# Kernel optimization log

Hardware: AMD Instinct MI355X
Metric: run time of the kernel (lower is better)

Reference implementation:

```python
import jax, jax.numpy as jnp
import numpy as np

N = 50000   # nodes
E = 800000  # edges (before self-loops)
G = 512     # graphs in batch
H = 4       # heads
C = 32      # hidden dim per head
NEG = 0.2   # LeakyReLU slope in GATConv
EPS = 1e-5  # BatchNorm eps


def setup_inputs():
    k = jax.random.split(jax.random.key(0), 32)
    f = lambda i, s: 0.1 * jax.random.normal(k[i], s, dtype=jnp.float32)
    inp = {
        "x": jax.random.normal(k[0], (N, 4), dtype=jnp.float32),
        "edge_index": jax.random.randint(k[1], (2, E), 0, N, dtype=jnp.int32),
        "batch": ((jnp.arange(N) * G) // N).astype(jnp.int32),  # sorted, every graph non-empty
        "u": jax.random.normal(k[2], (G, 10), dtype=jnp.float32),
    }
    dims = [(4, H * C, H, H * C), (H * C, H * C, H, H * C), (H * C, C, 1, C)]
    j = 3
    for l, (din, dout, hh, dbn) in enumerate(dims):
        inp[f"W{l}"] = f(j, (din, dout)); j += 1
        inp[f"a_src{l}"] = f(j, (hh, C)); j += 1
        inp[f"a_dst{l}"] = f(j, (hh, C)); j += 1
        inp[f"b{l}"] = f(j, (dbn,)); j += 1
        inp[f"bn_g{l}"] = 1.0 + f(j, (dbn,)); j += 1
        inp[f"bn_b{l}"] = f(j, (dbn,)); j += 1
        inp[f"bn_m{l}"] = f(j, (dbn,)); j += 1
        inp[f"bn_v{l}"] = 1.0 + 0.1 * jax.random.uniform(k[j], (dbn,), dtype=jnp.float32); j += 1
    inp["l1w"] = f(j, (2 * C + 10, C)); j += 1
    inp["l1b"] = f(j, (C,)); j += 1
    inp["l2w"] = f(j, (C, 1)); j += 1
    inp["l2b"] = f(j, (1,)); j += 1
    return inp


def gat(x, src, dst, W, a_s, a_d, b, heads, ch, concat):
    n = x.shape[0]
    h = (x @ W).reshape(n, heads, ch)                                   # [N,H,C]
    al_s = jnp.einsum('nhc,hc->nh', h, a_s)
    al_d = jnp.einsum('nhc,hc->nh', h, a_d)
    e = jax.nn.leaky_relu(al_s[src] + al_d[dst], NEG)                   # [E',H]
    m = jax.ops.segment_max(e, dst, num_segments=n)                     # per-dst softmax
    p = jnp.exp(e - m[dst])
    alpha = p / (jax.ops.segment_sum(p, dst, num_segments=n)[dst] + 1e-16)
    out = jax.ops.segment_sum(h[src] * alpha[:, :, None], dst, num_segments=n)
    out = out.reshape(n, heads * ch) if concat else out.mean(axis=1)
    return out + b


def bn(x, g, b, m, v):  # eval-mode BatchNorm1d
    return (x - m) * jax.lax.rsqrt(v + EPS) * g + b


def reference(x, edge_index, batch, u,
              W0, a_src0, a_dst0, b0, bn_g0, bn_b0, bn_m0, bn_v0,
              W1, a_src1, a_dst1, b1, bn_g1, bn_b1, bn_m1, bn_v1,
              W2, a_src2, a_dst2, b2, bn_g2, bn_b2, bn_m2, bn_v2,
              l1w, l1b, l2w, l2b):
    loops = jnp.arange(N, dtype=edge_index.dtype)  # GATConv add_self_loops=True
    src = jnp.concatenate([edge_index[0], loops])
    dst = jnp.concatenate([edge_index[1], loops])
    x = jax.nn.elu(bn(gat(x, src, dst, W0, a_src0, a_dst0, b0, H, C, True), bn_g0, bn_b0, bn_m0, bn_v0))
    x = jax.nn.elu(bn(gat(x, src, dst, W1, a_src1, a_dst1, b1, H, C, True), bn_g1, bn_b1, bn_m1, bn_v1))
    x = jax.nn.elu(bn(gat(x, src, dst, W2, a_src2, a_dst2, b2, 1, C, False), bn_g2, bn_b2, bn_m2, bn_v2))
    cnt = jax.ops.segment_sum(jnp.ones((N,), x.dtype), batch, num_segments=G)
    x_mean = jax.ops.segment_sum(x, batch, num_segments=G) / cnt[:, None]
    x_max = jax.ops.segment_max(x, batch, num_segments=G)
    comb = jnp.concatenate([x_mean, x_max, u], axis=1)                  # [G, 2C+10]
    hid = jax.nn.relu(comb @ l1w + l1b)
    return jax.nn.sigmoid(hid @ l2w + l2b)[:, 0]                        # [G]
```

## Files before the change

### kernel.cpp

```cpp
#include <hip/hip_runtime.h>
#include <hip/hip_bf16.h>
#include <math.h>

#define LRELU_NEG 0.2f
#define BN_EPS 1e-5f
#define CSR_SHIFT 7

typedef __attribute__((ext_vector_type(8))) short bf16x8;
typedef __attribute__((ext_vector_type(4))) float f32x4;

__device__ __forceinline__ float lrelu(float x) { return x > 0.f ? x : LRELU_NEG * x; }
__device__ __forceinline__ float b2f(__hip_bfloat16 v) { return __bfloat162float(v); }
__device__ __forceinline__ unsigned short f2bu(float v) {
  __hip_bfloat16 b = __float2bfloat16(v);
  return *(unsigned short*)&b;
}
__device__ __forceinline__ float blo(unsigned int u) { return __uint_as_float(u << 16); }
__device__ __forceinline__ float bhi(unsigned int u) { return __uint_as_float(u & 0xFFFF0000u); }
__device__ __forceinline__ float elu_fast(float v) { return v > 0.f ? v : __expf(v) - 1.f; }
__device__ __forceinline__ float ldw(const void* p, int i, int fl) {
  return fl ? b2f(((const __hip_bfloat16*)p)[i]) : ((const float*)p)[i];
}

__global__ __launch_bounds__(256) void k_setup(const int* __restrict__ ei, int E, int EN, int ebks,
                                               const unsigned short* __restrict__ w, int wn,
                                               int* __restrict__ flag, int* __restrict__ ph) {
  int b = blockIdx.x;
  int tid = threadIdx.x;
  if (b == ebks) {
    __shared__ int bad_s;
    if (tid == 0) bad_s = 0;
    __syncthreads();
    int bad = 0;
    for (int i = 2 * tid; i < wn; i += 512) {
      unsigned short u = w[i];
      if ((u & 0x7FFF) == 0) continue;
      int ex = (u >> 7) & 0xFF;
      if (ex > 131 || ex < 90) bad++;
    }
    atomicAdd(&bad_s, bad);
    __syncthreads();
    if (tid == 0) *flag = (bad_s < 2048) ? 1 : 0;
    return;
  }
  __shared__ int hist[512];
  hist[tid] = 0; hist[tid + 256] = 0;
  __syncthreads();
  int base = b * 4096;
  for (int i = 0; i < 16; i++) {
    int e = base + i * 256 + tid;
    if (e < EN) {
      int dst = (e < E) ? ei[E + e] : (e - E);
      atomicAdd(&hist[dst >> CSR_SHIFT], 1);
    }
  }
  __syncthreads();
  ph[b * 512 + tid] = hist[tid];
  ph[b * 512 + tid + 256] = hist[tid + 256];
}

__global__ __launch_bounds__(512) void k_bucketscan(const int* __restrict__ ph, int ebks,
                                                    int* __restrict__ bbase, int* __restrict__ gcursor) {
  __shared__ int wpre[8];
  int tid = threadIdx.x, lane = tid & 63, wid = tid >> 6;
  int v = 0;
  for (int i = 0; i < ebks; i++) v += ph[i * 512 + tid];
  int x = v;
  #pragma unroll
  for (int off = 1; off < 64; off <<= 1) {
    int y = __shfl_up(x, off);
    if (lane >= off) x += y;
  }
  if (lane == 63) wpre[wid] = x;
  __syncthreads();
  if (tid == 0) {
    int acc = 0;
    #pragma unroll
    for (int w = 0; w < 8; w++) { int t = wpre[w]; wpre[w] = acc; acc += t; }
  }
  __syncthreads();
  int excl = wpre[wid] + x - v;
  bbase[tid] = excl;
  gcursor[tid] = excl;
  if (tid == 511) bbase[512] = excl + v;
}

__global__ __launch_bounds__(256) void k_binscatter(const int* __restrict__ ei, int* __restrict__ gcursor,
                                                    unsigned int* __restrict__ pairs, int E, int EN) {
  __shared__ int cnt[512];
  __shared__ int base[512];
  int tid = threadIdx.x;
  cnt[tid] = 0; cnt[tid + 256] = 0;
  __syncthreads();
  int eb = blockIdx.x * 4096;
  int srcs[16], dsts[16];
  #pragma unroll
  for (int i = 0; i < 16; i++) {
    int e = eb + i * 256 + tid;
    srcs[i] = -1; dsts[i] = 0;
    if (e < EN) {
      int s, d;
      if (e < E) { s = ei[e]; d = ei[E + e]; } else { s = e - E; d = s; }
      srcs[i] = s; dsts[i] = d;
      atomicAdd(&cnt[d >> CSR_SHIFT], 1);
    }
  }
  __syncthreads();
  for (int b = tid; b < 512; b += 256) {
    int c = cnt[b];
    base[b] = c ? atomicAdd(&gcursor[b], c) : 0;
    cnt[b] = 0;
  }
  __syncthreads();
  #pragma unroll
  for (int i = 0; i < 16; i++) {
    if (srcs[i] >= 0) {
      int b = dsts[i] >> CSR_SHIFT;
      int loc = atomicAdd(&cnt[b], 1);
      pairs[base[b] + loc] = ((unsigned int)srcs[i] << CSR_SHIFT) | (unsigned int)(dsts[i] & 127);
    }
  }
}

__global__ __launch_bounds__(256) void k_csrfin(const unsigned int* __restrict__ pairs,
                                                const int* __restrict__ bbase,
                                                int* __restrict__ rs, int* __restrict__ col,
                                                int N, int EN) {
  __shared__ int dcount[128];
  __shared__ int wsum;
  __shared__ int lcur[128];
  int b = blockIdx.x, tid = threadIdx.x;
  if (tid < 128) dcount[tid] = 0;
  __syncthreads();
  int s = bbase[b], e = bbase[b + 1];
  for (int i = s + tid; i < e; i += 256)
    atomicAdd(&dcount[pairs[i] & 127], 1);
  __syncthreads();
  int x = 0, v = 0, wid = 0;
  if (tid < 128) {
    v = dcount[tid];
    int lane = tid & 63; wid = tid >> 6;
    x = v;
    #pragma unroll
    for (int off = 1; off < 64; off <<= 1) {
      int y = __shfl_up(x, off);
      if (lane >= off) x += y;
    }
    if (wid == 0 && lane == 63) wsum = x;
  }
  __syncthreads();
  if (tid < 128) {
    int excl = x - v + (wid ? wsum : 0);
    int r = s + excl;
    int node = (b << CSR_SHIFT) + tid;
    if (node < N) rs[node] = r;
    lcur[tid] = r;
  }
  if (b == 0 && tid == 0) rs[N] = EN;
  __syncthreads();
  for (int i = s + tid; i < e; i += 256) {
    unsigned int p = pairs[i];
    int pos = atomicAdd(&lcur[p & 127], 1);
    col[pos] = (int)(p >> CSR_SHIFT);
  }
}

struct FoldArgs {
  const void *W0, *as0, *ad0, *W1, *as1, *ad1, *W2, *as2, *ad2;
  const void *bn[15];
  float* W0p; __hip_bfloat16* Wt1; __hip_bfloat16* Wt2;
  float *A0, *B0, *A1, *B1, *A2, *B2;
};

__global__ __launch_bounds__(256) void k_foldW(FoldArgs fa, const int* __restrict__ flag) {
  int idx = blockIdx.x * 256 + threadIdx.x;
  int fl = *flag;
  if (idx < 576) {
    int k = idx / 144, c = idx % 144;
    float v = 0.f;
    if (c < 128) v = ldw(fa.W0, k * 128 + c, fl);
    else if (c < 136) {
      int hh = (c - 128) & 3; const void* a = (c < 132) ? fa.as0 : fa.ad0;
      float s = 0.f;
      for (int cc = 0; cc < 32; cc++)
        s += ldw(fa.W0, k * 128 + hh * 32 + cc, fl) * ldw(a, hh * 32 + cc, fl);
      v = s;
    }
    fa.W0p[k * 144 + c] = v;
    return;
  }
  idx -= 576;
  if (idx < 144 * 128) {
    int c = idx >> 7, k = idx & 127;
    float v = 0.f;
    if (c < 128) v = ldw(fa.W1, k * 128 + c, fl);
    else if (c < 136) {
      int hh = (c - 128) & 3; const void* a = (c < 132) ? fa.as1 : fa.ad1;
      float s = 0.f;
      for (int cc = 0; cc < 32; cc++)
        s += ldw(fa.W1, k * 128 + hh * 32 + cc, fl) * ldw(a, hh * 32 + cc, fl);
      v = s;
    }
    fa.Wt1[c * 128 + k] = __float2bfloat16(v);
    return;
  }
  idx -= 144 * 128;
  if (idx < 48 * 128) {
    int c = idx >> 7, k = idx & 127;
    float v = 0.f;
    if (c < 32) v = ldw(fa.W2, k * 32 + c, fl);
    else if (c == 32) { float s = 0.f; for (int cc = 0; cc < 32; cc++) s += ldw(fa.W2, k * 32 + cc, fl) * ldw(fa.as2, cc, fl); v = s; }
    else if (c == 33) { float s = 0.f; for (int cc = 0; cc < 32; cc++) s += ldw(fa.W2, k * 32 + cc, fl) * ldw(fa.ad2, cc, fl); v = s; }
    fa.Wt2[c * 128 + k] = __float2bfloat16(v);
    return;
  }
  idx -= 48 * 128;
  if (idx < 128) {
    float A = ldw(fa.bn[1], idx, fl) * rsqrtf(ldw(fa.bn[4], idx, fl) + BN_EPS);
    fa.A0[idx] = A;
    fa.B0[idx] = (ldw(fa.bn[0], idx, fl) - ldw(fa.bn[3], idx, fl)) * A + ldw(fa.bn[2], idx, fl);
    return;
  }
  idx -= 128;
  if (idx < 128) {
    float A = ldw(fa.bn[6], idx, fl) * rsqrtf(ldw(fa.bn[9], idx, fl) + BN_EPS);
    fa.A1[idx] = A;
    fa.B1[idx] = (ldw(fa.bn[5], idx, fl) - ldw(fa.bn[8], idx, fl)) * A + ldw(fa.bn[7], idx, fl);
    return;
  }
  idx -= 128;
  if (idx < 32) {
    float A = ldw(fa.bn[11], idx, fl) * rsqrtf(ldw(fa.bn[14], idx, fl) + BN_EPS);
    fa.A2[idx] = A;
    fa.B2[idx] = (ldw(fa.bn[10], idx, fl) - ldw(fa.bn[13], idx, fl)) * A + ldw(fa.bn[12], idx, fl);
  }
}

__global__ __launch_bounds__(256) void k_gemm0(const void* __restrict__ x, const float* __restrict__ W0p,
    const int* __restrict__ flag,
    __hip_bfloat16* __restrict__ h, float* __restrict__ als, float* __restrict__ ald, int N) {
  int t = blockIdx.x * 256 + threadIdx.x;
  int nrow = t / 36, cg = t - nrow * 36;
  if (nrow >= N) return;
  float4 xv;
  if (*flag) {
    uint2 tv = ((const uint2*)x)[nrow];
    xv = make_float4(blo(tv.x), bhi(tv.x), blo(tv.y), bhi(tv.y));
  } else {
    xv = ((const float4*)x)[nrow];
  }
  int c0 = cg * 4;
  float o[4];
  #pragma unroll
  for (int j = 0; j < 4; j++) {
    int c = c0 + j;
    o[j] = fmaf(xv.x, W0p[c], fmaf(xv.y, W0p[144 + c], fmaf(xv.z, W0p[288 + c], xv.w * W0p[432 + c])));
  }
  if (c0 < 128) {
    uint2 pk;
    pk.x = ((unsigned int)f2bu(o[1]) << 16) | f2bu(o[0]);
    pk.y = ((unsigned int)f2bu(o[3]) << 16) | f2bu(o[2]);
    *((uint2*)((unsigned short*)h + (size_t)nrow * 128) + cg) = pk;
  } else if (c0 == 128) {
    *(float4*)(als + (size_t)nrow * 4) = make_float4(o[0], o[1], o[2], o[3]);
  } else {
    *(float4*)(ald + (size_t)nrow * 4) = make_float4(o[0], o[1], o[2], o[3]);
  }
}

template <int CT, int DOUT, int HEADS>
__global__ __launch_bounds__(256) void k_mm(const __hip_bfloat16* __restrict__ xa,
    const __hip_bfloat16* __restrict__ Wt,
    __hip_bfloat16* __restrict__ h, float* __restrict__ als, float* __restrict__ ald, int N) {
  __shared__ unsigned short A_s[64 * 128];
  __shared__ unsigned short B_s[CT * 16 * 128];
  int tid = threadIdx.x;
  int row0 = blockIdx.x * 64;

  for (int i = tid; i < 1024; i += 256) {
    int r = i >> 4, slot = i & 15;
    int gr = row0 + r;
    float4 v = make_float4(0.f, 0.f, 0.f, 0.f);
    if (gr < N) v = ((const float4*)(xa + (size_t)gr * 128))[slot];
    *(float4*)((char*)A_s + r * 256 + ((slot ^ (r & 7)) << 4)) = v;
  }
  for (int i = tid; i < CT * 256; i += 256) {
    int r = i >> 4, slot = i & 15;
    float4 v = ((const float4*)Wt)[i];
    *(float4*)((char*)B_s + r * 256 + ((slot ^ (r & 7)) << 4)) = v;
  }
  __syncthreads();

  int l = tid & 63, w = tid >> 6;
  int lr = l & 15, lg = l >> 4;
  f32x4 acc[CT];
  #pragma unroll
  for (int ct = 0; ct < CT; ct++) acc[ct] = (f32x4){0.f, 0.f, 0.f, 0.f};

  int rA = w * 16 + lr;
  #pragma unroll
  for (int k0 = 0; k0 < 4; k0++) {
    int slot = k0 * 4 + lg;
    bf16x8 a = *(const bf16x8*)((const char*)A_s + rA * 256 + ((slot ^ (rA & 7)) << 4));
    #pragma unroll
    for (int ct = 0; ct < CT; ct++) {
      int rB = ct * 16 + lr;
      bf16x8 b = *(const bf16x8*)((const char*)B_s + rB * 256 + ((slot ^ (rB & 7)) << 4));
      acc[ct] = __builtin_amdgcn_mfma_f32_16x16x32_bf16(a, b, acc[ct], 0, 0, 0);
    }
  }

  #pragma unroll
  for (int ct = 0; ct < CT; ct++) {
    #pragma unroll
    for (int j = 0; j < 4; j++) {
      int gr = row0 + w * 16 + lg * 4 + j;
      if (gr >= N) continue;
      int col = ct * 16 + lr;
      float v = acc[ct][j];
      if (col < DOUT)                 h[(size_t)gr * DOUT + col] = __float2bfloat16(v);
      else if (col < DOUT + HEADS)    als[(size_t)gr * HEADS + (col - DOUT)] = v;
      else if (col < DOUT + 2*HEADS)  ald[(size_t)gr * HEADS + (col - DOUT - HEADS)] = v;
    }
  }
}

__global__ __launch_bounds__(256) void k_agg4(const __hip_bfloat16* __restrict__ h, const float* __restrict__ als,
    const float* __restrict__ ald, const int* __restrict__ rs, const int* __restrict__ col,
    const float* __restrict__ Aarr, const float* __restrict__ Barr,
    __hip_bfloat16* __restrict__ out, int N) {
  __shared__ int svs[8][32];
  __shared__ float ps[8][32][4];
  int tid = threadIdx.x;
  int sub = tid & 31, gi = tid >> 5;
  int n = blockIdx.x * 8 + gi;
  if (n >= N) return;
  int row = rs[n], deg = rs[n + 1] - row;
  float4 ad4 = *(const float4*)(ald + (size_t)n * 4);
  int hh2 = sub >> 3;
  float acc0 = 0.f, acc1 = 0.f, acc2 = 0.f, acc3 = 0.f;
  float s0 = 0.f, s1 = 0.f, s2 = 0.f, s3 = 0.f;

  for (int base = 0; base < deg; base += 32) {
    int k = base + sub;
    int sv = 0; float q0 = 0.f, q1 = 0.f, q2 = 0.f, q3 = 0.f;
    if (k < deg) {
      sv = col[row + k];
      float4 a4 = *(const float4*)(als + (size_t)sv * 4);
      q0 = __expf(lrelu(a4.x + ad4.x));
      q1 = __expf(lrelu(a4.y + ad4.y));
      q2 = __expf(lrelu(a4.z + ad4.z));
      q3 = __expf(lrelu(a4.w + ad4.w));
    }
    svs[gi][sub] = sv;
    *(float4*)&ps[gi][sub][0] = make_float4(q0, q1, q2, q3);
    s0 += q0; s1 += q1; s2 += q2; s3 += q3;
    int cnt = min(32, deg - base);
    int e = 0;
    for (; e + 3 < cnt; e += 4) {
      float pA = ps[gi][e][hh2];     int sA = svs[gi][e];
      float pB = ps[gi][e + 1][hh2]; int sB = svs[gi][e + 1];
      float pC = ps[gi][e + 2][hh2]; int sC = svs[gi][e + 2];
      float pD = ps[gi][e + 3][hh2]; int sD = svs[gi][e + 3];
      uint2 hA = *((const uint2*)(h + (size_t)sA * 128) + sub);
      uint2 hB = *((const uint2*)(h + (size_t)sB * 128) + sub);
      uint2 hC = *((const uint2*)(h + (size_t)sC * 128) + sub);
      uint2 hD = *((const uint2*)(h + (size_t)sD * 128) + sub);
      acc0 = fmaf(pA, blo(hA.x), acc0); acc1 = fmaf(pA, bhi(hA.x), acc1);
      acc2 = fmaf(pA, blo(hA.y), acc2); acc3 = fmaf(pA, bhi(hA.y), acc3);
      acc0 = fmaf(pB, blo(hB.x), acc0); acc1 = fmaf(pB, bhi(hB.x), acc1);
      acc2 = fmaf(pB, blo(hB.y), acc2); acc3 = fmaf(pB, bhi(hB.y), acc3);
      acc0 = fmaf(pC, blo(hC.x), acc0); acc1 = fmaf(pC, bhi(hC.x), acc1);
      acc2 = fmaf(pC, blo(hC.y), acc2); acc3 = fmaf(pC, bhi(hC.y), acc3);
      acc0 = fmaf(pD, blo(hD.x), acc0); acc1 = fmaf(pD, bhi(hD.x), acc1);
      acc2 = fmaf(pD, blo(hD.y), acc2); acc3 = fmaf(pD, bhi(hD.y), acc3);
    }
    for (; e < cnt; e++) {
      float pA = ps[gi][e][hh2]; int sA = svs[gi][e];
      uint2 hA = *((const uint2*)(h + (size_t)sA * 128) + sub);
      acc0 = fmaf(pA, blo(hA.x), acc0); acc1 = fmaf(pA, bhi(hA.x), acc1);
      acc2 = fmaf(pA, blo(hA.y), acc2); acc3 = fmaf(pA, bhi(hA.y), acc3);
    }
  }
  #pragma unroll
  for (int off = 1; off < 32; off <<= 1) {
    s0 += __shfl_xor(s0, off); s1 += __shfl_xor(s1, off);
    s2 += __shfl_xor(s2, off); s3 += __shfl_xor(s3, off);
  }
  float ssel = hh2 == 0 ? s0 : hh2 == 1 ? s1 : hh2 == 2 ? s2 : s3;
  float inv = 1.f / (ssel + 1e-16f);

  int c0 = 4 * sub;
  float4 Av = *(const float4*)(Aarr + c0);
  float4 Bv = *(const float4*)(Barr + c0);
  float v0 = acc0 * inv * Av.x + Bv.x;
  float v1 = acc1 * inv * Av.y + Bv.y;
  float v2 = acc2 * inv * Av.z + Bv.z;
  float v3 = acc3 * inv * Av.w + Bv.w;
  v0 = elu_fast(v0); v1 = elu_fast(v1); v2 = elu_fast(v2); v3 = elu_fast(v3);
  uint2 packed;
  packed.x = ((unsigned int)f2bu(v1) << 16) | f2bu(v0);
  packed.y = ((unsigned int)f2bu(v3) << 16) | f2bu(v2);
  *((uint2*)((unsigned short*)out + (size_t)n * 128) + sub) = packed;
}

__global__ __launch_bounds__(256) void k_agg1pool(const __hip_bfloat16* __restrict__ h,
    const float* __restrict__ als, const float* __restrict__ ald,
    const int* __restrict__ rs, const int* __restrict__ col,
    const float* __restrict__ A2, const float* __restrict__ B2,
    const int* __restrict__ batch,
    const void* __restrict__ u, const void* __restrict__ l1w, const void* __restrict__ l1b,
    const void* __restrict__ l2w, const void* __restrict__ l2b, const int* __restrict__ flag,
    float* __restrict__ out, int N, int G) {
  __shared__ int svs[16][16];
  __shared__ float ps[16][16];
  __shared__ float rsum[16][32];
  __shared__ float rmax[16][32];
  __shared__ float comb[74];
  int g = blockIdx.x;
  int tid = threadIdx.x, sub = tid & 15, gi = tid >> 4;
  int lo = 0, hi = N;
  while (lo < hi) { int mid = (lo + hi) >> 1; if (batch[mid] < g) lo = mid + 1; else hi = mid; }
  int start = lo;
  hi = N;
  while (lo < hi) { int mid = (lo + hi) >> 1; if (batch[mid] < g + 1) lo = mid + 1; else hi = mid; }
  int end = lo;

  float2 Af = *(const float2*)(A2 + 2 * sub);
  float2 Bf = *(const float2*)(B2 + 2 * sub);
  float sum0 = 0.f, sum1 = 0.f, mx0 = -1e30f, mx1 = -1e30f;

  for (int n = start + gi; n < end; n += 16) {
    int row = rs[n], deg = rs[n + 1] - row;
    float ad = ald[n];
    float acc0 = 0.f, acc1 = 0.f, s = 0.f;
    for (int base = 0; base < deg; base += 16) {
      int k = base + sub;
      int sv = 0; float q = 0.f;
      if (k < deg) {
        sv = col[row + k];
        q = __expf(lrelu(als[sv] + ad));
      }
      svs[gi][sub] = sv;
      ps[gi][sub] = q;
      s += q;
      int cnt = min(16, deg - base);
      int e = 0;
      for (; e + 3 < cnt; e += 4) {
        float pA = ps[gi][e];     int sA = svs[gi][e];
        float pB = ps[gi][e + 1]; int sB = svs[gi][e + 1];
        float pC = ps[gi][e + 2]; int sC = svs[gi][e + 2];
        float pD = ps[gi][e + 3]; int sD = svs[gi][e + 3];
        unsigned int hA = *((const unsigned int*)(h + (size_t)sA * 32) + sub);
        unsigned int hB = *((const unsigned int*)(h + (size_t)sB * 32) + sub);
        unsigned int hC = *((const unsigned int*)(h + (size_t)sC * 32) + sub);
        unsigned int hD = *((const unsigned int*)(h + (size_t)sD * 32) + sub);
        acc0 = fmaf(pA, blo(hA), acc0); acc1 = fmaf(pA, bhi(hA), acc1);
        acc0 = fmaf(pB, blo(hB), acc0); acc1 = fmaf(pB, bhi(hB), acc1);
        acc0 = fmaf(pC, blo(hC), acc0); acc1 = fmaf(pC, bhi(hC), acc1);
        acc0 = fmaf(pD, blo(hD), acc0); acc1 = fmaf(pD, bhi(hD), acc1);
      }
      for (; e < cnt; e++) {
        float pA = ps[gi][e]; int sA = svs[gi][e];
        unsigned int hA = *((const unsigned int*)(h + (size_t)sA * 32) + sub);
        acc0 = fmaf(pA, blo(hA), acc0); acc1 = fmaf(pA, bhi(hA), acc1);
      }
    }
    #pragma unroll
    for (int off = 1; off < 16; off <<= 1) s += __shfl_xor(s, off);
    float inv = 1.f / (s + 1e-16f);
    float v0 = acc0 * inv * Af.x + Bf.x;
    float v1 = acc1 * inv * Af.y + Bf.y;
    v0 = elu_fast(v0);
    v1 = elu_fast(v1);
    sum0 += v0; sum1 += v1;
    mx0 = fmaxf(mx0, v0); mx1 = fmaxf(mx1, v1);
  }
  rsum[gi][2 * sub] = sum0; rsum[gi][2 * sub + 1] = sum1;
  rmax[gi][2 * sub] = mx0;  rmax[gi][2 * sub + 1] = mx1;
  __syncthreads();
  int fl = *flag;
  if (tid < 32) {
    float s = 0.f, m = -1e30f;
    #pragma unroll
    for (int i = 0; i < 16; i++) { s += rsum[i][tid]; m = fmaxf(m, rmax[i][tid]); }
    float cnt = (float)(end - start);
    comb[tid] = s / cnt;
    comb[32 + tid] = m;
  }
  if (tid < 10) comb[64 + tid] = ldw(u, g * 10 + tid, fl);
  __syncthreads();
  if (tid < 32) {
    float acc = ldw(l1b, tid, fl);
    #pragma unroll
    for (int k = 0; k < 74; k++) acc = fmaf(comb[k], ldw(l1w, k * 32 + tid, fl), acc);
    acc = fmaxf(acc, 0.f);
    float v = acc * ldw(l2w, tid, fl);
    #pragma unroll
    for (int off = 16; off; off >>= 1) v += __shfl_xor(v, off, 32);
    if (tid == 0) out[g] = 1.f / (1.f + __expf(-(v + ldw(l2b, 0, fl))));
  }
}

extern "C" void kernel_launch(void* const* d_in, const int* in_sizes, int n_in,
                              void* d_out, int out_size, void* d_ws, size_t ws_size,
                              hipStream_t stream) {
  const int* EI    = (const int*)d_in[1];
  const int* BATCH = (const int*)d_in[2];
  float* OUT = (float*)d_out;

  int N = in_sizes[2];
  int E = in_sizes[1] / 2;
  int G = in_sizes[3] / 10;
  int EN = E + N;
  int NB = (N + 127) >> 7;
  int ebks = (EN + 4095) / 4096;

  char* ws = (char*)d_ws;
  size_t off = 0;
  auto alloc = [&](size_t bytes) {
    void* p = ws + off;
    off = (off + bytes + 255) & ~(size_t)255;
    return p;
  };
  __hip_bfloat16* f_xa = (__hip_bfloat16*)alloc((size_t)N * 128 * 2);
  __hip_bfloat16* f_h  = (__hip_bfloat16*)alloc((size_t)N * 128 * 2);
  float* f_als = (float*)alloc((size_t)N * 4 * 4);
  float* f_ald = (float*)alloc((size_t)N * 4 * 4);
  float* fW0p  = (float*)alloc(576 * 4);
  __hip_bfloat16* fWt1 = (__hip_bfloat16*)alloc(144 * 128 * 2);
  __hip_bfloat16* fWt2 = (__hip_bfloat16*)alloc(48 * 128 * 2);
  float* fA0 = (float*)alloc(128 * 4);
  float* fB0 = (float*)alloc(128 * 4);
  float* fA1 = (float*)alloc(128 * 4);
  float* fB1 = (float*)alloc(128 * 4);
  float* fA2 = (float*)alloc(32 * 4);
  float* fB2 = (float*)alloc(32 * 4);
  int* i_rs   = (int*)alloc((size_t)(N + 1) * 4);
  int* i_col  = (int*)alloc((size_t)EN * 4);
  unsigned int* i_pairs = (unsigned int*)alloc((size_t)EN * 4);
  int* i_ph      = (int*)alloc((size_t)ebks * 512 * 4);
  int* i_bbase   = (int*)alloc(513 * 4);
  int* i_gcursor = (int*)alloc(512 * 4);
  int* i_flag = (int*)alloc(256);

  k_setup<<<ebks + 1, 256, 0, stream>>>(EI, E, EN, ebks,
                                        (const unsigned short*)d_in[12], in_sizes[12],
                                        i_flag, i_ph);
  FoldArgs fa;
  fa.W0 = d_in[4];  fa.as0 = d_in[5];  fa.ad0 = d_in[6];
  fa.W1 = d_in[12]; fa.as1 = d_in[13]; fa.ad1 = d_in[14];
  fa.W2 = d_in[20]; fa.as2 = d_in[21]; fa.ad2 = d_in[22];
  for (int i = 0; i < 5; i++) {
    fa.bn[i]      = d_in[7 + i];
    fa.bn[5 + i]  = d_in[15 + i];
    fa.bn[10 + i] = d_in[23 + i];
  }
  fa.W0p = fW0p; fa.Wt1 = fWt1; fa.Wt2 = fWt2;
  fa.A0 = fA0; fa.B0 = fB0; fa.A1 = fA1; fa.B1 = fB1; fa.A2 = fA2; fa.B2 = fB2;
  k_foldW<<<100, 256, 0, stream>>>(fa, i_flag);

  k_bucketscan<<<1, 512, 0, stream>>>(i_ph, ebks, i_bbase, i_gcursor);
  k_binscatter<<<ebks, 256, 0, stream>>>(EI, i_gcursor, i_pairs, E, EN);
  k_csrfin<<<NB, 256, 0, stream>>>(i_pairs, i_bbase, i_rs, i_col, N, EN);

  k_gemm0<<<(N * 36 + 255) / 256, 256, 0, stream>>>(d_in[0], fW0p, i_flag, f_h, f_als, f_ald, N);
  k_agg4<<<(N + 7) / 8, 256, 0, stream>>>(f_h, f_als, f_ald, i_rs, i_col, fA0, fB0, f_xa, N);
  k_mm<9, 128, 4><<<(N + 63) / 64, 256, 0, stream>>>(f_xa, fWt1, f_h, f_als, f_ald, N);
  k_agg4<<<(N + 7) / 8, 256, 0, stream>>>(f_h, f_als, f_ald, i_rs, i_col, fA1, fB1, f_xa, N);
  k_mm<3, 32, 1><<<(N + 63) / 64, 256, 0, stream>>>(f_xa, fWt2, f_h, f_als, f_ald, N);
  k_agg1pool<<<G, 256, 0, stream>>>(f_h, f_als, f_ald, i_rs, i_col, fA2, fB2,
                                    BATCH, d_in[3], d_in[28], d_in[29], d_in[30], d_in[31],
                                    i_flag, OUT, N, G);
}
```

Measured before the change: 216.0 us.

## Split last-layer aggregation from graph pooling into separate kernels

The fused per-graph kernel did layer-3 attention aggregation and pooling in one block per graph, which gave only 512 blocks of work. The change moves aggregation into a per-node kernel (16 nodes per block) that writes bf16 activations. A small 64-thread per-graph kernel then reduces mean and max with shuffles and runs the MLP head. This adds a kernel launch and an intermediate write and read of N×32 bf16 values in exchange for far more parallelism in the aggregation step.

```diff
diff --git a/kernel.cpp b/kernel.cpp
--- a/kernel.cpp
+++ b/kernel.cpp
@@ -404,101 +404,112 @@
   *((uint2*)((unsigned short*)out + (size_t)n * 128) + sub) = packed;
 }
 
-__global__ __launch_bounds__(256) void k_agg1pool(const __hip_bfloat16* __restrict__ h,
-    const float* __restrict__ als, const float* __restrict__ ald,
-    const int* __restrict__ rs, const int* __restrict__ col,
+__global__ __launch_bounds__(256) void k_agg1(const __hip_bfloat16* __restrict__ h, const float* __restrict__ als,
+    const float* __restrict__ ald, const int* __restrict__ rs, const int* __restrict__ col,
     const float* __restrict__ A2, const float* __restrict__ B2,
-    const int* __restrict__ batch,
-    const void* __restrict__ u, const void* __restrict__ l1w, const void* __restrict__ l1b,
-    const void* __restrict__ l2w, const void* __restrict__ l2b, const int* __restrict__ flag,
-    float* __restrict__ out, int N, int G) {
+    __hip_bfloat16* __restrict__ out, int N) {
   __shared__ int svs[16][16];
   __shared__ float ps[16][16];
-  __shared__ float rsum[16][32];
-  __shared__ float rmax[16][32];
-  __shared__ float comb[74];
+  int tid = threadIdx.x;
+  int sub = tid & 15, gi = tid >> 4;
+  int n = blockIdx.x * 16 + gi;
+  if (n >= N) return;
+  int row = rs[n], deg = rs[n + 1] - row;
+  float ad = ald[n];
+  float acc0 = 0.f, acc1 = 0.f, s = 0.f;
+
+  for (int base = 0; base < deg; base += 16) {
+    int k = base + sub;
+    int sv = 0; float q = 0.f;
+    if (k < deg) {
+      sv = col[row + k];
+      q = __expf(lrelu(als[sv] + ad));
+    }
+    svs[gi][sub] = sv;
+    ps[gi][sub] = q;
+    s += q;
+    int cnt = min(16, deg - base);
+    int e = 0;
+    for (; e + 3 < cnt; e += 4) {
+      float pA = ps[gi][e];     int sA = svs[gi][e];
+      float pB = ps[gi][e + 1]; int sB = svs[gi][e + 1];
+      float pC = ps[gi][e + 2]; int sC = svs[gi][e + 2];
+      float pD = ps[gi][e + 3]; int sD = svs[gi][e + 3];
+      unsigned int hA = *((const unsigned int*)(h + (size_t)sA * 32) + sub);
+      unsigned int hB = *((const unsigned int*)(h + (size_t)sB * 32) + sub);
+      unsigned int hC = *((const unsigned int*)(h + (size_t)sC * 32) + sub);
+      unsigned int hD = *((const unsigned int*)(h + (size_t)sD * 32) + sub);
+      acc0 = fmaf(pA, blo(hA), acc0); acc1 = fmaf(pA, bhi(hA), acc1);
+      acc0 = fmaf(pB, blo(hB), acc0); acc1 = fmaf(pB, bhi(hB), acc1);
+      acc0 = fmaf(pC, blo(hC), acc0); acc1 = fmaf(pC, bhi(hC), acc1);
+      acc0 = fmaf(pD, blo(hD), acc0); acc1 = fmaf(pD, bhi(hD), acc1);
+    }
+    for (; e < cnt; e++) {
+      float pA = ps[gi][e]; int sA = svs[gi][e];
+      unsigned int hA = *((const unsigned int*)(h + (size_t)sA * 32) + sub);
+      acc0 = fmaf(pA, blo(hA), acc0); acc1 = fmaf(pA, bhi(hA), acc1);
+    }
+  }
+  #pragma unroll
+  for (int off = 1; off < 16; off <<= 1) s += __shfl_xor(s, off);
+  float inv = 1.f / (s + 1e-16f);
+
+  int c0 = 2 * sub;
+  float2 Af = *(const float2*)(A2 + c0);
+  float2 Bf = *(const float2*)(B2 + c0);
+  float v0 = acc0 * inv * Af.x + Bf.x;
+  float v1 = acc1 * inv * Af.y + Bf.y;
+  v0 = elu_fast(v0);
+  v1 = elu_fast(v1);
+  unsigned int packed = ((unsigned int)f2bu(v1) << 16) | f2bu(v0);
+  *((unsigned int*)((unsigned short*)out + (size_t)n * 32) + sub) = packed;
+}
+
+__global__ __launch_bounds__(64) void k_pool(const __hip_bfloat16* __restrict__ x3, const int* __restrict__ batch,
+    const void* __restrict__ u, const void* __restrict__ l1w,
+    const void* __restrict__ l1b, const void* __restrict__ l2w,
+    const void* __restrict__ l2b, const int* __restrict__ flag,
+    float* __restrict__ out, int N, int G) {
   int g = blockIdx.x;
-  int tid = threadIdx.x, sub = tid & 15, gi = tid >> 4;
+  int lane = threadIdx.x;
   int lo = 0, hi = N;
   while (lo < hi) { int mid = (lo + hi) >> 1; if (batch[mid] < g) lo = mid + 1; else hi = mid; }
   int start = lo;
   hi = N;
   while (lo < hi) { int mid = (lo + hi) >> 1; if (batch[mid] < g + 1) lo = mid + 1; else hi = mid; }
   int end = lo;
-
-  float2 Af = *(const float2*)(A2 + 2 * sub);
-  float2 Bf = *(const float2*)(B2 + 2 * sub);
+  int sub = lane & 15, q = lane >> 4;
   float sum0 = 0.f, sum1 = 0.f, mx0 = -1e30f, mx1 = -1e30f;
-
-  for (int n = start + gi; n < end; n += 16) {
-    int row = rs[n], deg = rs[n + 1] - row;
-    float ad = ald[n];
-    float acc0 = 0.f, acc1 = 0.f, s = 0.f;
-    for (int base = 0; base < deg; base += 16) {
-      int k = base + sub;
-      int sv = 0; float q = 0.f;
-      if (k < deg) {
-        sv = col[row + k];
-        q = __expf(lrelu(als[sv] + ad));
-      }
-      svs[gi][sub] = sv;
-      ps[gi][sub] = q;
-      s += q;
-      int cnt = min(16, deg - base);
-      int e = 0;
-      for (; e + 3 < cnt; e += 4) {
-        float pA = ps[gi][e];     int sA = svs[gi][e];
-        float pB = ps[gi][e + 1]; int sB = svs[gi][e + 1];
-        float pC = ps[gi][e + 2]; int sC = svs[gi][e + 2];
-        float pD = ps[gi][e + 3]; int sD = svs[gi][e + 3];
-        unsigned int hA = *((const unsigned int*)(h + (size_t)sA * 32) + sub);
-        unsigned int hB = *((const unsigned int*)(h + (size_t)sB * 32) + sub);
-        unsigned int hC = *((const unsigned int*)(h + (size_t)sC * 32) + sub);
-        unsigned int hD = *((const unsigned int*)(h + (size_t)sD * 32) + sub);
-        acc0 = fmaf(pA, blo(hA), acc0); acc1 = fmaf(pA, bhi(hA), acc1);
-        acc0 = fmaf(pB, blo(hB), acc0); acc1 = fmaf(pB, bhi(hB), acc1);
-        acc0 = fmaf(pC, blo(hC), acc0); acc1 = fmaf(pC, bhi(hC), acc1);
-        acc0 = fmaf(pD, blo(hD), acc0); acc1 = fmaf(pD, bhi(hD), acc1);
-      }
-      for (; e < cnt; e++) {
-        float pA = ps[gi][e]; int sA = svs[gi][e];
-        unsigned int hA = *((const unsigned int*)(h + (size_t)sA * 32) + sub);
-        acc0 = fmaf(pA, blo(hA), acc0); acc1 = fmaf(pA, bhi(hA), acc1);
-      }
-    }
-    #pragma unroll
-    for (int off = 1; off < 16; off <<= 1) s += __shfl_xor(s, off);
-    float inv = 1.f / (s + 1e-16f);
-    float v0 = acc0 * inv * Af.x + Bf.x;
-    float v1 = acc1 * inv * Af.y + Bf.y;
-    v0 = elu_fast(v0);
-    v1 = elu_fast(v1);
+  for (int i = start + q; i < end; i += 4) {
+    unsigned int hv = *((const unsigned int*)(x3 + (size_t)i * 32) + sub);
+    float v0 = blo(hv), v1 = bhi(hv);
     sum0 += v0; sum1 += v1;
     mx0 = fmaxf(mx0, v0); mx1 = fmaxf(mx1, v1);
   }
-  rsum[gi][2 * sub] = sum0; rsum[gi][2 * sub + 1] = sum1;
-  rmax[gi][2 * sub] = mx0;  rmax[gi][2 * sub + 1] = mx1;
-  __syncthreads();
+  sum0 += __shfl_xor(sum0, 16); sum0 += __shfl_xor(sum0, 32);
+  sum1 += __shfl_xor(sum1, 16); sum1 += __shfl_xor(sum1, 32);
+  mx0 = fmaxf(mx0, __shfl_xor(mx0, 16)); mx0 = fmaxf(mx0, __shfl_xor(mx0, 32));
+  mx1 = fmaxf(mx1, __shfl_xor(mx1, 16)); mx1 = fmaxf(mx1, __shfl_xor(mx1, 32));
+  __shared__ float comb[74];
   int fl = *flag;
-  if (tid < 32) {
-    float s = 0.f, m = -1e30f;
+  if (lane < 16) {
+    float cnt = (float)(end - start);
+    comb[2 * lane] = sum0 / cnt;
+    comb[2 * lane + 1] = sum1 / cnt;
+    comb[32 + 2 * lane] = mx0;
+    comb[32 + 2 * lane + 1] = mx1;
+  }
+  if (lane < 10) comb[64 + lane] = ldw(u, g * 10 + lane, fl);
+  __syncthreads();
+  if (lane < 32) {
+    float acc = ldw(l1b, lane, fl);
     #pragma unroll
-    for (int i = 0; i < 16; i++) { s += rsum[i][tid]; m = fmaxf(m, rmax[i][tid]); }
-    float cnt = (float)(end - start);
-    comb[tid] = s / cnt;
-    comb[32 + tid] = m;
-  }
-  if (tid < 10) comb[64 + tid] = ldw(u, g * 10 + tid, fl);
-  __syncthreads();
-  if (tid < 32) {
-    float acc = ldw(l1b, tid, fl);
-    #pragma unroll
-    for (int k = 0; k < 74; k++) acc = fmaf(comb[k], ldw(l1w, k * 32 + tid, fl), acc);
+    for (int k = 0; k < 74; k++) acc = fmaf(comb[k], ldw(l1w, k * 32 + lane, fl), acc);
     acc = fmaxf(acc, 0.f);
-    float v = acc * ldw(l2w, tid, fl);
+    float v = acc * ldw(l2w, lane, fl);
     #pragma unroll
     for (int off = 16; off; off >>= 1) v += __shfl_xor(v, off, 32);
-    if (tid == 0) out[g] = 1.f / (1.f + __expf(-(v + ldw(l2b, 0, fl))));
+    if (lane == 0) out[g] = 1.f / (1.f + __expf(-(v + ldw(l2b, 0, fl))));
   }
 }
 
@@ -569,7 +580,8 @@
   k_mm<9, 128, 4><<<(N + 63) / 64, 256, 0, stream>>>(f_xa, fWt1, f_h, f_als, f_ald, N);
   k_agg4<<<(N + 7) / 8, 256, 0, stream>>>(f_h, f_als, f_ald, i_rs, i_col, fA1, fB1, f_xa, N);
   k_mm<3, 32, 1><<<(N + 63) / 64, 256, 0, stream>>>(f_xa, fWt2, f_h, f_als, f_ald, N);
-  k_agg1pool<<<G, 256, 0, stream>>>(f_h, f_als, f_ald, i_rs, i_col, fA2, fB2,
-                                    BATCH, d_in[3], d_in[28], d_in[29], d_in[30], d_in[31],
-                                    i_flag, OUT, N, G);
-}
+  k_agg1<<<(N + 15) / 16, 256, 0, stream>>>(f_h, f_als, f_ald, i_rs, i_col, fA2, fB2, f_xa, N);
+
+  k_pool<<<G, 64, 0, stream>>>(f_xa, BATCH, d_in[3], d_in[28], d_in[29], d_in[30], d_in[31],
+                               i_flag, OUT, N, G);
+}
```

Result: faster. 211.3 us (-2.2%).
